# Kernel optimization log

Measured on AMD Instinct MI355X. Metric: run time of the kernel, lower is better.

The kernel has to match this reference:

```python
import jax, jax.numpy as jnp
import numpy as np

B, T, E, H, L = 524288, 1, 64, 32, 5  # batch, seq_len (forced to 1 by fc1 shape), embed_dim, hidden_size, num_layers


def setup_inputs() -> dict:
    key = jax.random.key(0)
    ks = jax.random.split(key, 9)
    s = 0.1  # weight init scale
    return {
        "x": jax.random.normal(ks[0], (B, T, E), jnp.float32),
        "w_ih0": jax.random.normal(ks[1], (4 * H, E), jnp.float32) * s,   # layer 0 input weights
        "w_hh0": jax.random.normal(ks[2], (4 * H, H), jnp.float32) * s,
        "w_ih_rest": jax.random.normal(ks[3], (L - 1, 4 * H, H), jnp.float32) * s,
        "w_hh_rest": jax.random.normal(ks[4], (L - 1, 4 * H, H), jnp.float32) * s,
        "b_ih": jax.random.normal(ks[5], (L, 4 * H), jnp.float32) * s,
        "b_hh": jax.random.normal(ks[6], (L, 4 * H), jnp.float32) * s,
        "fc_w": jax.random.normal(ks[7], (E, T * H), jnp.float32) * s,   # Linear(hidden_size, embed_dim)
        "fc_b": jax.random.normal(ks[8], (E,), jnp.float32) * s,
    }


def _lstm_layer(xs, w_ih, w_hh, b_ih, b_hh):
    # xs: (T, Bn, in_dim); PyTorch gate order: i, f, g, o
    Bn = xs.shape[1]
    h0 = jnp.zeros((Bn, H), xs.dtype)
    c0 = jnp.zeros((Bn, H), xs.dtype)

    def step(carry, x):
        h, c = carry
        gates = x @ w_ih.T + h @ w_hh.T + (b_ih + b_hh)  # (Bn, 4H)
        i, f, g, o = jnp.split(gates, 4, axis=-1)
        c = jax.nn.sigmoid(f) * c + jax.nn.sigmoid(i) * jnp.tanh(g)
        h = jax.nn.sigmoid(o) * jnp.tanh(c)
        return (h, c), h

    _, ys = jax.lax.scan(step, (h0, c0), xs)
    return ys  # (T, Bn, H)


def reference(x, w_ih0, w_hh0, w_ih_rest, w_hh_rest, b_ih, b_hh, fc_w, fc_b):
    xs = jnp.swapaxes(x, 0, 1)  # (T, B, E), batch_first -> time-major for scan
    ys = _lstm_layer(xs, w_ih0, w_hh0, b_ih[0], b_hh[0])
    for l in range(L - 1):
        ys = _lstm_layer(ys, w_ih_rest[l], w_hh_rest[l], b_ih[l + 1], b_hh[l + 1])
    out = jnp.swapaxes(ys, 0, 1).reshape(x.shape[0], -1)  # (B, T*H)
    return out @ fc_w.T + fc_b  # (B, E)
```

## Files before the change

### kernel.cpp

```cpp
#include <hip/hip_runtime.h>


typedef float    f32x4 __attribute__((ext_vector_type(4)));
typedef _Float16 h16x8 __attribute__((ext_vector_type(8)));


#define LOG2E   1.4426950408889634f

__device__ __forceinline__ float lstm_act(float gi, float gg, float go) {
    float a  = __builtin_amdgcn_exp2f(gi);
    float b  = __builtin_amdgcn_exp2f(gg);
    float cc = (1.0f - b) * __builtin_amdgcn_rcpf((1.0f + a) * (1.0f + b));
    float z  = cc * cc;
    float N  = __builtin_fmaf(z, z + 105.0f, 945.0f);
    float D  = __builtin_fmaf(z, __builtin_fmaf(z, 15.0f, 420.0f), 945.0f);
    float d  = __builtin_amdgcn_exp2f(go);
    return (cc * N) * __builtin_amdgcn_rcpf((1.0f + d) * D);
}

__global__ void prep_kernel(const float* __restrict__ w_ih0,
                            const float* __restrict__ w_ih_rest,
                            const float* __restrict__ b_ih,
                            const float* __restrict__ b_hh,
                            const float* __restrict__ fc_w,
                            const float* __restrict__ fc_b,
                            unsigned char* __restrict__ ws)
{
    int t = blockIdx.x * 256 + threadIdx.x;
    if (t < 80 * 64) {
        int f = t >> 6, lane = t & 63;
        int q = lane >> 4, c = lane & 15;
        int layer, ntile, kfrag, s;
        if (f < 24)      { layer = 0;          ntile = f >> 2;        kfrag = (f >> 1) & 1; s = f & 1; }
        else if (f < 72) { int r = f - 24;     layer = 1 + r / 12; r %= 12;
                           ntile = r >> 1;     kfrag = 0;             s = r & 1; }
        else             { int r = f - 72;     layer = 5;
                           ntile = r >> 1;     kfrag = 0;             s = r & 1; }
        int kbase = kfrag * 32 + q * 8;
        const float* src;
        float scale;
        if (layer <= 4) {
            int n = ntile * 16 + c;
            int orig = n + (n < 32 ? 0 : 32);
            scale = (n >= 32 && n < 64) ? -2.0f * LOG2E : -LOG2E;
            src = (layer == 0) ? (w_ih0 + orig * 64 + kbase)
                               : (w_ih_rest + (((layer - 1) * 128) + orig) * 32 + kbase);
        } else {
            int n = 4 * c + ntile;
            scale = 1.0f;
            src = fc_w + n * 32 + kbase;
        }
        h16x8 outv;
        #pragma unroll
        for (int j = 0; j < 8; j++) {
            float v = src[j] * scale;
            _Float16 hi = (_Float16)v;
            outv[j] = (s == 0) ? hi : (_Float16)(v - (float)hi);
        }
        ((h16x8*)ws)[f * 64 + lane] = outv;
    } else if (t < 80 * 64 + 480) {
        int idx = t - 80 * 64;
        int l = idx / 96, r = idx % 96;
        int orig = r + (r < 32 ? 0 : 32);
        float scale = (r >= 32 && r < 64) ? -2.0f * LOG2E : -LOG2E;
        float* bias = (float*)(ws + 81920);
        bias[idx] = (b_ih[l * 128 + orig] + b_hh[l * 128 + orig]) * scale;
    } else if (t < 80 * 64 + 480 + 64) {
        int e = t - (80 * 64 + 480);
        float* fcb = (float*)(ws + 83840);
        fcb[e] = fc_b[e];
    }
}

__global__ __launch_bounds__(256)
void lstm_mfma(const float* __restrict__ x,
               const unsigned char* __restrict__ ws,
               float* __restrict__ out)
{
    __shared__ __attribute__((aligned(16))) _Float16 hs[4][32][40];

    const int tid  = threadIdx.x;
    const int wave = tid >> 6;
    const int lane = tid & 63;
    const int q    = lane >> 4;
    const int c    = lane & 15;

    const long batch_base = ((long)blockIdx.x * 4 + wave) * 32;

    const h16x8* wfrag = (const h16x8*)ws;
    const float* biasf = (const float*)(ws + 81920);
    const float* fcbf  = (const float*)(ws + 83840);

    h16x8 xh[2][2];
    #pragma unroll
    for (int s = 0; s < 2; s++) {
        const float4* xp = (const float4*)(x + (batch_base + s * 16 + c) * 64);
        #pragma unroll
        for (int kf = 0; kf < 2; kf++) {
            float4 a = xp[kf * 8 + q * 2];
            float4 b = xp[kf * 8 + q * 2 + 1];
            float v[8] = {a.x, a.y, a.z, a.w, b.x, b.y, b.z, b.w};
            #pragma unroll
            for (int j = 0; j < 8; j++) xh[s][kf][j] = (_Float16)v[j];
        }
    }

    #pragma unroll 1
    for (int g2 = 0; g2 < 2; g2++) {
        f32x4 acc[3][2];
        #pragma unroll
        for (int kind = 0; kind < 3; kind++) {
            float bv = biasf[kind * 32 + g2 * 16 + c];
            #pragma unroll
            for (int s = 0; s < 2; s++) acc[kind][s] = (f32x4){bv, bv, bv, bv};
        }
        #pragma unroll
        for (int kind = 0; kind < 3; kind++) {
            int nt = kind * 2 + g2;
            #pragma unroll
            for (int kf = 0; kf < 2; kf++) {
                int fr = (nt * 2 + kf) * 2;
                h16x8 wh = wfrag[fr * 64 + lane];
                h16x8 wl = wfrag[fr * 64 + 64 + lane];
                #pragma unroll
                for (int s = 0; s < 2; s++) {
                    acc[kind][s] = __builtin_amdgcn_mfma_f32_16x16x32_f16(xh[s][kf], wh, acc[kind][s], 0, 0, 0);
                    acc[kind][s] = __builtin_amdgcn_mfma_f32_16x16x32_f16(xh[s][kf], wl, acc[kind][s], 0, 0, 0);
                }
            }
        }
        #pragma unroll
        for (int s = 0; s < 2; s++) {
            #pragma unroll
            for (int r = 0; r < 4; r++) {
                float hv = lstm_act(acc[0][s][r], acc[1][s][r], acc[2][s][r]);
                hs[wave][s * 16 + q * 4 + r][g2 * 16 + c] = (_Float16)hv;
            }
        }
    }

    #pragma unroll 1
    for (int l = 1; l <= 4; l++) {
        __builtin_amdgcn_wave_barrier();
        h16x8 ah[2];
        #pragma unroll
        for (int s = 0; s < 2; s++)
            ah[s] = *(const h16x8*)&hs[wave][s * 16 + c][q * 8];
        __builtin_amdgcn_wave_barrier();
        #pragma unroll 1
        for (int g2 = 0; g2 < 2; g2++) {
            f32x4 acc[3][2];
            #pragma unroll
            for (int kind = 0; kind < 3; kind++) {
                float bv = biasf[l * 96 + kind * 32 + g2 * 16 + c];
                #pragma unroll
                for (int s = 0; s < 2; s++) acc[kind][s] = (f32x4){bv, bv, bv, bv};
            }
            #pragma unroll
            for (int kind = 0; kind < 3; kind++) {
                int fr = 24 + (l - 1) * 12 + (kind * 2 + g2) * 2;
                h16x8 wh = wfrag[fr * 64 + lane];
                h16x8 wl = wfrag[fr * 64 + 64 + lane];
                #pragma unroll
                for (int s = 0; s < 2; s++) {
                    acc[kind][s] = __builtin_amdgcn_mfma_f32_16x16x32_f16(ah[s], wh, acc[kind][s], 0, 0, 0);
                    acc[kind][s] = __builtin_amdgcn_mfma_f32_16x16x32_f16(ah[s], wl, acc[kind][s], 0, 0, 0);
                }
            }
            #pragma unroll
            for (int s = 0; s < 2; s++) {
                #pragma unroll
                for (int r = 0; r < 4; r++) {
                    float hv = lstm_act(acc[0][s][r], acc[1][s][r], acc[2][s][r]);
                    hs[wave][s * 16 + q * 4 + r][g2 * 16 + c] = (_Float16)hv;
                }
            }
        }
    }

    __builtin_amdgcn_wave_barrier();
    h16x8 fh[2];
    #pragma unroll
    for (int s = 0; s < 2; s++)
        fh[s] = *(const h16x8*)&hs[wave][s * 16 + c][q * 8];

    f32x4 acc[4][2];
    #pragma unroll
    for (int t4 = 0; t4 < 4; t4++) {
        float bv = fcbf[4 * c + t4];
        #pragma unroll
        for (int s = 0; s < 2; s++) acc[t4][s] = (f32x4){bv, bv, bv, bv};
    }
    #pragma unroll
    for (int t4 = 0; t4 < 4; t4++) {
        int fr = 72 + t4 * 2;
        h16x8 wh = wfrag[fr * 64 + lane];
        h16x8 wl = wfrag[fr * 64 + 64 + lane];
        #pragma unroll
        for (int s = 0; s < 2; s++) {
            acc[t4][s] = __builtin_amdgcn_mfma_f32_16x16x32_f16(fh[s], wh, acc[t4][s], 0, 0, 0);
            acc[t4][s] = __builtin_amdgcn_mfma_f32_16x16x32_f16(fh[s], wl, acc[t4][s], 0, 0, 0);
        }
    }
    #pragma unroll
    for (int s = 0; s < 2; s++) {
        #pragma unroll
        for (int r = 0; r < 4; r++) {
            long row = batch_base + s * 16 + q * 4 + r;
            float4 o4 = {acc[0][s][r], acc[1][s][r], acc[2][s][r], acc[3][s][r]};
            *(float4*)(out + row * 64 + 4 * c) = o4;
        }
    }
}

extern "C" void kernel_launch(void* const* d_in, const int* in_sizes, int n_in,
                              void* d_out, int out_size, void* d_ws, size_t ws_size,
                              hipStream_t stream)
{
    const float* x         = (const float*)d_in[0];
    const float* w_ih0     = (const float*)d_in[1];
    const float* w_ih_rest = (const float*)d_in[3];
    const float* b_ih      = (const float*)d_in[5];
    const float* b_hh      = (const float*)d_in[6];
    const float* fc_w      = (const float*)d_in[7];
    const float* fc_b      = (const float*)d_in[8];
    unsigned char* ws      = (unsigned char*)d_ws;
    float* out             = (float*)d_out;

    prep_kernel<<<23, 256, 0, stream>>>(w_ih0, w_ih_rest, b_ih, b_hh, fc_w, fc_b, ws);

    lstm_mfma<<<4096, 256, 0, stream>>>(x, ws, out);
}
```

Baseline: 299.3 us.

## Drop fp16 hi/lo weight split and process 64 rows per wave

Weights were stored as fp16 hi plus lo residual pairs to emulate higher precision, which doubled the MFMA count. They are now a single fp16 copy, halving the matrix work and the weight fragment loads. Each wave also handles 64 batch rows instead of 32, so each weight fragment load is reused across more MFMAs and the grid is halved. The risks are lower accuracy from single-fp16 weights and higher register pressure from the larger accumulator arrays, which may reduce occupancy.

```diff
diff --git a/kernel.cpp b/kernel.cpp
--- a/kernel.cpp
+++ b/kernel.cpp
@@ -27,15 +27,13 @@
                             unsigned char* __restrict__ ws)
 {
     int t = blockIdx.x * 256 + threadIdx.x;
-    if (t < 80 * 64) {
+    if (t < 40 * 64) {
         int f = t >> 6, lane = t & 63;
         int q = lane >> 4, c = lane & 15;
-        int layer, ntile, kfrag, s;
-        if (f < 24)      { layer = 0;          ntile = f >> 2;        kfrag = (f >> 1) & 1; s = f & 1; }
-        else if (f < 72) { int r = f - 24;     layer = 1 + r / 12; r %= 12;
-                           ntile = r >> 1;     kfrag = 0;             s = r & 1; }
-        else             { int r = f - 72;     layer = 5;
-                           ntile = r >> 1;     kfrag = 0;             s = r & 1; }
+        int layer, ntile, kfrag;
+        if (f < 12)      { layer = 0;      ntile = f >> 1;  kfrag = f & 1; }
+        else if (f < 36) { int r = f - 12; layer = 1 + r / 6; ntile = r % 6; kfrag = 0; }
+        else             { layer = 5;      ntile = f - 36;  kfrag = 0; }
         int kbase = kfrag * 32 + q * 8;
         const float* src;
         float scale;
@@ -52,22 +50,18 @@
         }
         h16x8 outv;
         #pragma unroll
-        for (int j = 0; j < 8; j++) {
-            float v = src[j] * scale;
-            _Float16 hi = (_Float16)v;
-            outv[j] = (s == 0) ? hi : (_Float16)(v - (float)hi);
-        }
+        for (int j = 0; j < 8; j++) outv[j] = (_Float16)(src[j] * scale);
         ((h16x8*)ws)[f * 64 + lane] = outv;
-    } else if (t < 80 * 64 + 480) {
-        int idx = t - 80 * 64;
+    } else if (t < 40 * 64 + 480) {
+        int idx = t - 40 * 64;
         int l = idx / 96, r = idx % 96;
         int orig = r + (r < 32 ? 0 : 32);
         float scale = (r >= 32 && r < 64) ? -2.0f * LOG2E : -LOG2E;
-        float* bias = (float*)(ws + 81920);
+        float* bias = (float*)(ws + 40960);
         bias[idx] = (b_ih[l * 128 + orig] + b_hh[l * 128 + orig]) * scale;
-    } else if (t < 80 * 64 + 480 + 64) {
-        int e = t - (80 * 64 + 480);
-        float* fcb = (float*)(ws + 83840);
+    } else if (t < 40 * 64 + 480 + 64) {
+        int e = t - (40 * 64 + 480);
+        float* fcb = (float*)(ws + 42880);
         fcb[e] = fc_b[e];
     }
 }
@@ -77,7 +71,7 @@
                const unsigned char* __restrict__ ws,
                float* __restrict__ out)
 {
-    __shared__ __attribute__((aligned(16))) _Float16 hs[4][32][40];
+    __shared__ __attribute__((aligned(16))) _Float16 hs[4][64][40];
 
     const int tid  = threadIdx.x;
     const int wave = tid >> 6;
@@ -85,52 +79,48 @@
     const int q    = lane >> 4;
     const int c    = lane & 15;
 
-    const long batch_base = ((long)blockIdx.x * 4 + wave) * 32;
+    const long batch_base = ((long)blockIdx.x * 4 + wave) * 64;
 
     const h16x8* wfrag = (const h16x8*)ws;
-    const float* biasf = (const float*)(ws + 81920);
-    const float* fcbf  = (const float*)(ws + 83840);
-
-    h16x8 xh[2][2];
-    #pragma unroll
-    for (int s = 0; s < 2; s++) {
+    const float* biasf = (const float*)(ws + 40960);
+    const float* fcbf  = (const float*)(ws + 42880);
+
+    h16x8 xh[4][2];
+    #pragma unroll
+    for (int s = 0; s < 4; s++) {
         const float4* xp = (const float4*)(x + (batch_base + s * 16 + c) * 64);
         #pragma unroll
         for (int kf = 0; kf < 2; kf++) {
             float4 a = xp[kf * 8 + q * 2];
             float4 b = xp[kf * 8 + q * 2 + 1];
-            float v[8] = {a.x, a.y, a.z, a.w, b.x, b.y, b.z, b.w};
-            #pragma unroll
-            for (int j = 0; j < 8; j++) xh[s][kf][j] = (_Float16)v[j];
+            xh[s][kf][0] = (_Float16)a.x; xh[s][kf][1] = (_Float16)a.y;
+            xh[s][kf][2] = (_Float16)a.z; xh[s][kf][3] = (_Float16)a.w;
+            xh[s][kf][4] = (_Float16)b.x; xh[s][kf][5] = (_Float16)b.y;
+            xh[s][kf][6] = (_Float16)b.z; xh[s][kf][7] = (_Float16)b.w;
         }
     }
 
     #pragma unroll 1
     for (int g2 = 0; g2 < 2; g2++) {
-        f32x4 acc[3][2];
+        f32x4 acc[3][4];
         #pragma unroll
         for (int kind = 0; kind < 3; kind++) {
             float bv = biasf[kind * 32 + g2 * 16 + c];
             #pragma unroll
-            for (int s = 0; s < 2; s++) acc[kind][s] = (f32x4){bv, bv, bv, bv};
+            for (int s = 0; s < 4; s++) acc[kind][s] = (f32x4){bv, bv, bv, bv};
         }
         #pragma unroll
         for (int kind = 0; kind < 3; kind++) {
-            int nt = kind * 2 + g2;
             #pragma unroll
             for (int kf = 0; kf < 2; kf++) {
-                int fr = (nt * 2 + kf) * 2;
-                h16x8 wh = wfrag[fr * 64 + lane];
-                h16x8 wl = wfrag[fr * 64 + 64 + lane];
-                #pragma unroll
-                for (int s = 0; s < 2; s++) {
+                h16x8 wh = wfrag[((kind * 2 + g2) * 2 + kf) * 64 + lane];
+                #pragma unroll
+                for (int s = 0; s < 4; s++)
                     acc[kind][s] = __builtin_amdgcn_mfma_f32_16x16x32_f16(xh[s][kf], wh, acc[kind][s], 0, 0, 0);
-                    acc[kind][s] = __builtin_amdgcn_mfma_f32_16x16x32_f16(xh[s][kf], wl, acc[kind][s], 0, 0, 0);
-                }
-            }
-        }
-        #pragma unroll
-        for (int s = 0; s < 2; s++) {
+            }
+        }
+        #pragma unroll
+        for (int s = 0; s < 4; s++) {
             #pragma unroll
             for (int r = 0; r < 4; r++) {
                 float hv = lstm_act(acc[0][s][r], acc[1][s][r], acc[2][s][r]);
@@ -142,33 +132,29 @@
     #pragma unroll 1
     for (int l = 1; l <= 4; l++) {
         __builtin_amdgcn_wave_barrier();
-        h16x8 ah[2];
-        #pragma unroll
-        for (int s = 0; s < 2; s++)
+        h16x8 ah[4];
+        #pragma unroll
+        for (int s = 0; s < 4; s++)
             ah[s] = *(const h16x8*)&hs[wave][s * 16 + c][q * 8];
         __builtin_amdgcn_wave_barrier();
         #pragma unroll 1
         for (int g2 = 0; g2 < 2; g2++) {
-            f32x4 acc[3][2];
+            f32x4 acc[3][4];
             #pragma unroll
             for (int kind = 0; kind < 3; kind++) {
                 float bv = biasf[l * 96 + kind * 32 + g2 * 16 + c];
                 #pragma unroll
-                for (int s = 0; s < 2; s++) acc[kind][s] = (f32x4){bv, bv, bv, bv};
+                for (int s = 0; s < 4; s++) acc[kind][s] = (f32x4){bv, bv, bv, bv};
             }
             #pragma unroll
             for (int kind = 0; kind < 3; kind++) {
-                int fr = 24 + (l - 1) * 12 + (kind * 2 + g2) * 2;
-                h16x8 wh = wfrag[fr * 64 + lane];
-                h16x8 wl = wfrag[fr * 64 + 64 + lane];
-                #pragma unroll
-                for (int s = 0; s < 2; s++) {
+                h16x8 wh = wfrag[(12 + (l - 1) * 6 + kind * 2 + g2) * 64 + lane];
+                #pragma unroll
+                for (int s = 0; s < 4; s++)
                     acc[kind][s] = __builtin_amdgcn_mfma_f32_16x16x32_f16(ah[s], wh, acc[kind][s], 0, 0, 0);
-                    acc[kind][s] = __builtin_amdgcn_mfma_f32_16x16x32_f16(ah[s], wl, acc[kind][s], 0, 0, 0);
-                }
-            }
-            #pragma unroll
-            for (int s = 0; s < 2; s++) {
+            }
+            #pragma unroll
+            for (int s = 0; s < 4; s++) {
                 #pragma unroll
                 for (int r = 0; r < 4; r++) {
                     float hv = lstm_act(acc[0][s][r], acc[1][s][r], acc[2][s][r]);
@@ -179,35 +165,30 @@
     }
 
     __builtin_amdgcn_wave_barrier();
-    h16x8 fh[2];
-    #pragma unroll
-    for (int s = 0; s < 2; s++)
+    h16x8 fh[4];
+    #pragma unroll
+    for (int s = 0; s < 4; s++)
         fh[s] = *(const h16x8*)&hs[wave][s * 16 + c][q * 8];
 
-    f32x4 acc[4][2];
+    h16x8 w4[4];
+    float bv4[4];
     #pragma unroll
     for (int t4 = 0; t4 < 4; t4++) {
-        float bv = fcbf[4 * c + t4];
-        #pragma unroll
-        for (int s = 0; s < 2; s++) acc[t4][s] = (f32x4){bv, bv, bv, bv};
-    }
-    #pragma unroll
-    for (int t4 = 0; t4 < 4; t4++) {
-        int fr = 72 + t4 * 2;
-        h16x8 wh = wfrag[fr * 64 + lane];
-        h16x8 wl = wfrag[fr * 64 + 64 + lane];
-        #pragma unroll
-        for (int s = 0; s < 2; s++) {
-            acc[t4][s] = __builtin_amdgcn_mfma_f32_16x16x32_f16(fh[s], wh, acc[t4][s], 0, 0, 0);
-            acc[t4][s] = __builtin_amdgcn_mfma_f32_16x16x32_f16(fh[s], wl, acc[t4][s], 0, 0, 0);
-        }
-    }
-    #pragma unroll
-    for (int s = 0; s < 2; s++) {
+        w4[t4]  = wfrag[(36 + t4) * 64 + lane];
+        bv4[t4] = fcbf[4 * c + t4];
+    }
+    #pragma unroll
+    for (int s = 0; s < 4; s++) {
+        f32x4 a4[4];
+        #pragma unroll
+        for (int t4 = 0; t4 < 4; t4++) a4[t4] = (f32x4){bv4[t4], bv4[t4], bv4[t4], bv4[t4]};
+        #pragma unroll
+        for (int t4 = 0; t4 < 4; t4++)
+            a4[t4] = __builtin_amdgcn_mfma_f32_16x16x32_f16(fh[s], w4[t4], a4[t4], 0, 0, 0);
         #pragma unroll
         for (int r = 0; r < 4; r++) {
             long row = batch_base + s * 16 + q * 4 + r;
-            float4 o4 = {acc[0][s][r], acc[1][s][r], acc[2][s][r], acc[3][s][r]};
+            float4 o4 = {a4[0][r], a4[1][r], a4[2][r], a4[3][r]};
             *(float4*)(out + row * 64 + 4 * c) = o4;
         }
     }
@@ -227,7 +208,7 @@
     unsigned char* ws      = (unsigned char*)d_ws;
     float* out             = (float*)d_out;
 
-    prep_kernel<<<23, 256, 0, stream>>>(w_ih0, w_ih_rest, b_ih, b_hh, fc_w, fc_b, ws);
-
-    lstm_mfma<<<4096, 256, 0, stream>>>(x, ws, out);
-}
+    prep_kernel<<<13, 256, 0, stream>>>(w_ih0, w_ih_rest, b_ih, b_hh, fc_w, fc_b, ws);
+
+    lstm_mfma<<<2048, 256, 0, stream>>>(x, ws, out);
+}
```

Result: no change. 295.7 us (-1.2%).
